# Optimization experiments

Measured on AMD Instinct MI355X. Metric: run time of the kernel, lower is better.

Reference implementation:

```python
import jax, jax.numpy as jnp
import numpy as np

N = 131072        # total points
M = 34            # max_num_neighbors (hard-coded in forward)
K = 15            # kernel points (torch-points3d default for 3D KPConv)
C_IN, C_OUT = 32, 64
POINT_INFLUENCE = 0.04        # prev_grid_size * sigma
KERNEL_RADIUS = 1.5 * POINT_INFLUENCE  # _INFLUENCE_TO_RADIUS * point_influence
BN_EPS = 1e-5
NEG_SLOPE = 0.2


def setup_inputs() -> dict:
    key = jax.random.key(0)
    ks = jax.random.split(key, 6)
    # points in a [0, 0.1]^3 box so random neighbors can fall inside the influence radius
    xyz = jax.random.uniform(ks[0], (N, 3), jnp.float32) * 0.1
    feats = jax.random.normal(ks[1], (N, C_IN), jnp.float32)
    neighbor_idx = jax.random.randint(ks[2], (N, M), 0, N, dtype=jnp.int32)
    # fixed kernel-point disposition: points inside a sphere of radius KERNEL_RADIUS
    kp_dir = jax.random.normal(ks[3], (K, 3), jnp.float32)
    kp_dir = kp_dir / jnp.linalg.norm(kp_dir, axis=1, keepdims=True)
    kp_rad = jax.random.uniform(ks[4], (K, 1), jnp.float32) ** (1.0 / 3.0)
    k_points = kp_dir * kp_rad * KERNEL_RADIUS
    weight = jax.random.normal(ks[5], (K, C_IN, C_OUT), jnp.float32) / np.sqrt(K * C_IN)
    gamma = jnp.ones((C_OUT,), jnp.float32)
    beta = jnp.zeros((C_OUT,), jnp.float32)
    return {"xyz": xyz, "feats": feats, "neighbor_idx": neighbor_idx,
            "weight": weight, "k_points": k_points, "gamma": gamma, "beta": beta}


def _kpconv(xyz, feats, neighbor_idx, weight, k_points):
    # shadow point / shadow feature row for out-of-range neighbor index == N
    sup = jnp.concatenate([xyz, jnp.full((1, 3), 1e6, xyz.dtype)], axis=0)
    f = jnp.concatenate([feats, jnp.zeros((1, feats.shape[1]), feats.dtype)], axis=0)
    # [N, M, 3] neighbor offsets relative to each query point
    nb = sup[neighbor_idx] - xyz[:, None, :]
    # [N, M, K] distance from each neighbor to each kernel point
    diff = nb[:, :, None, :] - k_points[None, None, :, :]
    dist = jnp.sqrt(jnp.sum(diff * diff, axis=-1))
    # linear kernel influence, 'sum' aggregation
    w = jnp.maximum(0.0, 1.0 - dist / POINT_INFLUENCE)          # [N, M, K]
    nb_f = f[neighbor_idx]                                       # [N, M, C_IN]
    wf = jnp.einsum('nmk,nmc->nkc', w, nb_f)                     # [N, K, C_IN]
    return jnp.einsum('nkc,kcd->nd', wf, weight)                 # [N, C_OUT]


def reference(xyz, feats, neighbor_idx, weight, k_points, gamma, beta):
    out = _kpconv(xyz, feats, neighbor_idx, weight, k_points)
    # FastBatchNorm1d (training-mode batch statistics) + LeakyReLU(0.2)
    mean = jnp.mean(out, axis=0)
    var = jnp.mean((out - mean) ** 2, axis=0)
    out = (out - mean) * jax.lax.rsqrt(var + BN_EPS) * gamma + beta
    return jnp.where(out >= 0, out, NEG_SLOPE * out)
```

## Files before the change

### kernel.cpp

```cpp
#include <hip/hip_runtime.h>

#define NPTS 131072
#define MNBR 34
#define KP 15
#define CIN 32
#define COUT 64
#define INV_INFL 25.0f
#define BN_EPS 1e-5f
#define NEG_SLOPE 0.2f
#define PPB 16
#define NBLK (NPTS / PPB)
#define NBIN 512
#define SKIP_D2 0.01f

typedef unsigned short u16;
typedef unsigned int u32;
typedef short short8 __attribute__((ext_vector_type(8)));
typedef float f32x4 __attribute__((ext_vector_type(4)));

static __device__ __forceinline__ u16 f2bf(float f) {
    u32 x = __float_as_uint(f);
    x += 0x7fffu + ((x >> 16) & 1u);
    return (u16)(x >> 16);
}
static __device__ __forceinline__ u32 pk2bf(float lo, float hi) {
    u32 a = __float_as_uint(lo) + 0x8000u;
    u32 b = __float_as_uint(hi) + 0x8000u;
    return (a >> 16) | (b & 0xffff0000u);
}
static __device__ __forceinline__ float rdlanef(float v, int l) {
    return __uint_as_float(__builtin_amdgcn_readlane(__float_as_uint(v), l));
}

#define WS_WT   0u
#define WS_SCSH 65536u
#define WS_SP   131072u
#define WS_QP   262144u
#define WS_XY   393216u
#define WS_FB   2490624u

__global__ __launch_bounds__(256) void prep(const float* __restrict__ Wg,
                                            const float* __restrict__ feats,
                                            const float* __restrict__ xyz,
                                            u16* __restrict__ WT, float4* __restrict__ XY,
                                            u32* __restrict__ FBu, float* __restrict__ SpQp) {
    int b = blockIdx.x;
    if (b < 120) {
        int i2 = b * 256 + threadIdx.x;
        WT[(i2 & 63) * 480 + (i2 >> 6)] = f2bf(Wg[i2]);
    } else if (b < 633) {
        int r = (b - 120) * 256 + threadIdx.x;
        if (r <= NPTS) {
            float4 v;
            if (r < NPTS) v = make_float4(xyz[3 * r], xyz[3 * r + 1], xyz[3 * r + 2], 0.f);
            else          v = make_float4(1e6f, 1e6f, 1e6f, 0.f);
            XY[r] = v;
        }
    } else if (b < 8826) {
        int g = (b - 633) * 256 + threadIdx.x;
        if (g < ((NPTS + 1) * CIN) / 2) {
            int e = g * 2;
            u32 v = 0;
            if (e < NPTS * CIN)
                v = (u32)f2bf(feats[e]) | ((u32)f2bf(feats[e + 1]) << 16);
            FBu[g] = v;
        }
    } else {
        SpQp[(b - 8826) * 256 + threadIdx.x] = 0.f;
    }
}

__global__ __launch_bounds__(128, 3) void kpconv_conv(
    const float* __restrict__ xyz, const int* __restrict__ nbr,
    const float4* __restrict__ XY, const u32* __restrict__ FBu,
    const u16* __restrict__ WT, const float* __restrict__ kpts,
    float* __restrict__ out, float* __restrict__ Sp, float* __restrict__ Qp)
{
    __shared__ u32 wf[PPB * 256];
    __shared__ float4 offs4[2][2][64];

    const int tid = threadIdx.x, lane = tid & 63, wave = tid >> 6;
    const int q = lane >> 4, t = lane & 15;
    const int pbase = blockIdx.x * PPB + wave * 8;

    float axt = 0.f, ayt = 0.f, azt = 0.f, ckt = 1e30f;
    if (t < KP) {
        float kx = kpts[3 * t], ky = kpts[3 * t + 1], kz = kpts[3 * t + 2];
        axt = -2.f * kx; ayt = -2.f * ky; azt = -2.f * kz;
        ckt = fmaf(kx, kx, fmaf(ky, ky, kz * kz));
    }
    const int wslot = (lane & ~7) | ((lane ^ (lane >> 3)) & 7);
    const int sl = q * 8;

    auto ldnbr = [&](int pp) {
        int v = NPTS;
        if (lane < MNBR) v = nbr[(size_t)(pbase + pp) * MNBR + lane];
        if ((u32)v > (u32)NPTS) v = NPTS;
        return v;
    };

    float qxv[8], qyv[8], qzv[8];
    #pragma unroll
    for (int p = 0; p < 8; ++p) {
        const int n1 = pbase + p;
        qxv[p] = xyz[3 * n1]; qyv[p] = xyz[3 * n1 + 1]; qzv[p] = xyz[3 * n1 + 2];
    }

    u32 fbA[8] = {0,0,0,0,0,0,0,0};
    u32 fbB[8] = {0,0,0,0,0,0,0,0};
    u32 fbC[8] = {0,0,0,0,0,0,0,0};
    u32 d32A = 0, d33A = 0, d32B = 0, d33B = 0, d32N = 0, d33N = 0;

    int ix0 = ldnbr(0);
    int ix1 = ldnbr(1);
    int ixF = ldnbr(2);
    int ix3 = ldnbr(3);
    float4 pn0 = XY[ix0];
    float4 pn1 = XY[ix1];
    float4 pnF = XY[ixF];

    {
        float ox = pn0.x - qxv[0], oy = pn0.y - qyv[0], oz = pn0.z - qzv[0];
        float ow = fmaf(ox, ox, fmaf(oy, oy, oz * oz));
        offs4[wave][0][wslot] = make_float4(ox, oy, oz, ow);
        #pragma unroll
        for (int j = 0; j < 8; ++j) {
            float dj = __shfl(ow, sl + j, 64);
            u32 r0 = (u32)__shfl(ix0, sl + j, 64);
            if (dj < SKIP_D2) fbA[j] = FBu[(size_t)r0 * 16 + t];
        }
        float w32 = rdlanef(ow, 32), w33 = rdlanef(ow, 33);
        int r32 = __builtin_amdgcn_readlane(ix0, 32);
        int r33 = __builtin_amdgcn_readlane(ix0, 33);
        if (w32 < SKIP_D2) d32A = FBu[(size_t)r32 * 16 + t];
        if (w33 < SKIP_D2) d33A = FBu[(size_t)r33 * 16 + t];
    }
    float o1x, o1y, o1z, o1w;
    {
        o1x = pn1.x - qxv[1]; o1y = pn1.y - qyv[1]; o1z = pn1.z - qzv[1];
        o1w = fmaf(o1x, o1x, fmaf(o1y, o1y, o1z * o1z));
        #pragma unroll
        for (int j = 0; j < 8; ++j) {
            float dj = __shfl(o1w, sl + j, 64);
            u32 r1 = (u32)__shfl(ix1, sl + j, 64);
            if (dj < SKIP_D2) fbB[j] = FBu[(size_t)r1 * 16 + t];
        }
        float w32 = rdlanef(o1w, 32), w33 = rdlanef(o1w, 33);
        int r32 = __builtin_amdgcn_readlane(ix1, 32);
        int r33 = __builtin_amdgcn_readlane(ix1, 33);
        if (w32 < SKIP_D2) d32B = FBu[(size_t)r32 * 16 + t];
        if (w33 < SKIP_D2) d33B = FBu[(size_t)r33 * 16 + t];
    }

    #pragma unroll
    for (int p = 0; p < 8; ++p) {
        int ixN = NPTS;
        if (p < 4) ixN = ldnbr(p + 4);
        float4 pnN = make_float4(1e6f, 1e6f, 1e6f, 0.f);
        if (p < 5) pnN = XY[ix3];
        float o2x = 0.f, o2y = 0.f, o2z = 0.f, o2w = 1e30f;
        if (p < 6) {
            o2x = pnF.x - qxv[p + 2]; o2y = pnF.y - qyv[p + 2]; o2z = pnF.z - qzv[p + 2];
            o2w = fmaf(o2x, o2x, fmaf(o2y, o2y, o2z * o2z));
            #pragma unroll
            for (int j = 0; j < 8; ++j) {
                float dj = __shfl(o2w, sl + j, 64);
                u32 r2 = (u32)__shfl(ixF, sl + j, 64);
                if (dj < SKIP_D2) fbC[j] = FBu[(size_t)r2 * 16 + t];
            }
            float w32 = rdlanef(o2w, 32), w33 = rdlanef(o2w, 33);
            int r32 = __builtin_amdgcn_readlane(ixF, 32);
            int r33 = __builtin_amdgcn_readlane(ixF, 33);
            if (w32 < SKIP_D2) d32N = FBu[(size_t)r32 * 16 + t];
            if (w33 < SKIP_D2) d33N = FBu[(size_t)r33 * 16 + t];
        }
        if (p < 7) {
            offs4[wave][(p + 1) & 1][wslot] = make_float4(o1x, o1y, o1z, o1w);
        }

        const float4* ob = &offs4[wave][p & 1][0];
        float wj[8];
        #pragma unroll
        for (int j = 0; j < 8; ++j) {
            float4 o = ob[q * 8 + (j ^ q)];
            float d2 = fmaf(o.x, axt, fmaf(o.y, ayt, fmaf(o.z, azt, ckt))) + o.w;
            float dd = __builtin_amdgcn_sqrtf(d2);
            wj[j] = fmaxf(0.f, fmaf(dd, -INV_INFL, 1.f));
        }
        union { short8 v; u32 d[4]; } a1, a2, e1, o1, e2, o2;
        #pragma unroll
        for (int i = 0; i < 4; ++i) a1.d[i] = pk2bf(wj[2 * i], wj[2 * i + 1]);
        {
            float4 oA = ob[36], oB = ob[37];
            float dA = __builtin_amdgcn_sqrtf(fmaf(oA.x, axt, fmaf(oA.y, ayt, fmaf(oA.z, azt, ckt))) + oA.w);
            float dB = __builtin_amdgcn_sqrtf(fmaf(oB.x, axt, fmaf(oB.y, ayt, fmaf(oB.z, azt, ckt))) + oB.w);
            float wA = fmaxf(0.f, fmaf(dA, -INV_INFL, 1.f));
            float wB = fmaxf(0.f, fmaf(dB, -INV_INFL, 1.f));
            a2.d[0] = (q == 0) ? pk2bf(wA, wB) : 0u;
            a2.d[1] = 0; a2.d[2] = 0; a2.d[3] = 0;
        }
        #pragma unroll
        for (int i = 0; i < 4; ++i) {
            u32 aa = fbA[2 * i], bb2 = fbA[2 * i + 1];
            e1.d[i] = (aa & 0xffffu) | (bb2 << 16);
            o1.d[i] = (aa >> 16) | (bb2 & 0xffff0000u);
        }
        {
            u32 lo = (d32A & 0xffffu) | (d33A << 16);
            u32 hi = (d32A >> 16) | (d33A & 0xffff0000u);
            e2.d[0] = (q == 0) ? lo : 0u;  e2.d[1] = 0; e2.d[2] = 0; e2.d[3] = 0;
            o2.d[0] = (q == 0) ? hi : 0u;  o2.d[1] = 0; o2.d[2] = 0; o2.d[3] = 0;
        }
        f32x4 c0 = {0.f, 0.f, 0.f, 0.f}, c1 = {0.f, 0.f, 0.f, 0.f};
        c0 = __builtin_amdgcn_mfma_f32_16x16x32_bf16(a1.v, e1.v, c0, 0, 0, 0);
        c0 = __builtin_amdgcn_mfma_f32_16x16x32_bf16(a2.v, e2.v, c0, 0, 0, 0);
        c1 = __builtin_amdgcn_mfma_f32_16x16x32_bf16(a1.v, o1.v, c1, 0, 0, 0);
        c1 = __builtin_amdgcn_mfma_f32_16x16x32_bf16(a2.v, o2.v, c1, 0, 0, 0);

        const int row = wave * 8 + p;
        #pragma unroll
        for (int r = 0; r < 4; ++r) {
            int ko = q * 4 + r;
            u32 pk = pk2bf(c0[r], c1[r]);
            int unit = ko * 4 + (t >> 2);
            wf[row * 256 + ((unit ^ (row & 7)) << 2) + (t & 3)] = pk;
        }

        #pragma unroll
        for (int j = 0; j < 8; ++j) { fbA[j] = fbB[j]; fbB[j] = fbC[j]; }
        d32A = d32B; d33A = d33B; d32B = d32N; d33B = d33N;
        pnF = pnN; o1x = o2x; o1y = o2y; o1z = o2z; o1w = o2w;
        ixF = ix3; ix3 = ixN;
    }
    __syncthreads();

    const int wcol0 = (wave * 2 + 0) * 16 + t;
    const int wcol1 = (wave * 2 + 1) * 16 + t;
    f32x4 A0 = {0.f, 0.f, 0.f, 0.f}, A1 = {0.f, 0.f, 0.f, 0.f};
    const u16* wt0 = WT + wcol0 * 480 + q * 8;
    const u16* wt1 = WT + wcol1 * 480 + q * 8;
    #pragma unroll
    for (int ks = 0; ks < KP; ++ks) {
        const int u = ks * 4 + q;
        short8 a   = *(const short8*)&wf[t * 256 + ((u ^ (t & 7)) << 2)];
        short8 bb0 = *(const short8*)(wt0 + ks * 32);
        short8 bb1 = *(const short8*)(wt1 + ks * 32);
        A0 = __builtin_amdgcn_mfma_f32_16x16x32_bf16(a, bb0, A0, 0, 0, 0);
        A1 = __builtin_amdgcn_mfma_f32_16x16x32_bf16(a, bb1, A1, 0, 0, 0);
    }
    const int base = blockIdx.x * PPB;
    float s0 = 0.f, q0 = 0.f, s1 = 0.f, q1 = 0.f;
    #pragma unroll
    for (int r = 0; r < 4; ++r) {
        float v0 = A0[r], v1 = A1[r];
        out[(base + q * 4 + r) * COUT + wcol0] = v0;
        out[(base + q * 4 + r) * COUT + wcol1] = v1;
        s0 += v0; q0 = fmaf(v0, v0, q0);
        s1 += v1; q1 = fmaf(v1, v1, q1);
    }
    s0 += __shfl_xor(s0, 16, 64); s0 += __shfl_xor(s0, 32, 64);
    q0 += __shfl_xor(q0, 16, 64); q0 += __shfl_xor(q0, 32, 64);
    s1 += __shfl_xor(s1, 16, 64); s1 += __shfl_xor(s1, 32, 64);
    q1 += __shfl_xor(q1, 16, 64); q1 += __shfl_xor(q1, 32, 64);
    if (q == 0) {
        const int bin = blockIdx.x >> 4;
        atomicAdd(&Sp[wcol0 * NBIN + bin], s0);
        atomicAdd(&Qp[wcol0 * NBIN + bin], q0);
        atomicAdd(&Sp[wcol1 * NBIN + bin], s1);
        atomicAdd(&Qp[wcol1 * NBIN + bin], q1);
    }
}

__global__ __launch_bounds__(256) void bn_reduce(
    const float* __restrict__ Sp, const float* __restrict__ Qp,
    const float* __restrict__ gamma, const float* __restrict__ beta,
    float* __restrict__ scsh)
{
    const int ch = blockIdx.x;
    const int tid = threadIdx.x;
    float s = 0.f, qq = 0.f;
    if (tid < NBIN / 4) {
        float4 a = ((const float4*)(Sp + ch * NBIN))[tid]; s  = a.x + a.y + a.z + a.w;
        float4 b = ((const float4*)(Qp + ch * NBIN))[tid]; qq = b.x + b.y + b.z + b.w;
    }
    #pragma unroll
    for (int off = 1; off < 64; off <<= 1) {
        s += __shfl_xor(s, off, 64); qq += __shfl_xor(qq, off, 64);
    }
    __shared__ float red[8];
    const int w = tid >> 6;
    if ((tid & 63) == 0) { red[w * 2] = s; red[w * 2 + 1] = qq; }
    __syncthreads();
    if (tid == 0) {
        s  = red[0] + red[2] + red[4] + red[6];
        qq = red[1] + red[3] + red[5] + red[7];
        float mean = s * (1.0f / NPTS);
        float var  = qq * (1.0f / NPTS) - mean * mean;
        float sc = gamma[ch] * rsqrtf(var + BN_EPS);
        scsh[ch] = sc;
        scsh[64 + ch] = beta[ch] - mean * sc;
    }
}

__global__ __launch_bounds__(256) void bn_apply(
    float* __restrict__ out, const float* __restrict__ scsh)
{
    __shared__ float sc[64], sh[64];
    const int tid = threadIdx.x;
    if (tid < 64) { sc[tid] = scsh[tid]; sh[tid] = scsh[64 + tid]; }
    __syncthreads();
    const int gid = blockIdx.x * 256 + tid;
    float4 v = ((const float4*)out)[gid];
    const int c0 = (gid * 4) & 63;
    float y0 = fmaf(v.x, sc[c0 + 0], sh[c0 + 0]);
    float y1 = fmaf(v.y, sc[c0 + 1], sh[c0 + 1]);
    float y2 = fmaf(v.z, sc[c0 + 2], sh[c0 + 2]);
    float y3 = fmaf(v.w, sc[c0 + 3], sh[c0 + 3]);
    float4 w;
    w.x = fmaxf(y0, NEG_SLOPE * y0);
    w.y = fmaxf(y1, NEG_SLOPE * y1);
    w.z = fmaxf(y2, NEG_SLOPE * y2);
    w.w = fmaxf(y3, NEG_SLOPE * y3);
    ((float4*)out)[gid] = w;
}

extern "C" void kernel_launch(void* const* d_in, const int* in_sizes, int n_in,
                              void* d_out, int out_size, void* d_ws, size_t ws_size,
                              hipStream_t stream) {
    (void)in_sizes; (void)n_in; (void)out_size; (void)ws_size;
    const float* xyz   = (const float*)d_in[0];
    const float* feats = (const float*)d_in[1];
    const int*   nbr   = (const int*)d_in[2];
    const float* Wg    = (const float*)d_in[3];
    const float* kpts  = (const float*)d_in[4];
    const float* gamma = (const float*)d_in[5];
    const float* beta  = (const float*)d_in[6];
    float* out = (float*)d_out;
    char* ws = (char*)d_ws;
    u16*    WT   = (u16*)(ws + WS_WT);
    float*  scsh = (float*)(ws + WS_SCSH);
    float*  Sp   = (float*)(ws + WS_SP);
    float*  Qp   = (float*)(ws + WS_QP);
    float4* XY   = (float4*)(ws + WS_XY);
    u32*    FBu  = (u32*)(ws + WS_FB);

    prep<<<dim3(9082), dim3(256), 0, stream>>>(Wg, feats, xyz, WT, XY, FBu, Sp);
    kpconv_conv<<<dim3(NBLK), dim3(128), 0, stream>>>(xyz, nbr, XY, FBu, WT, kpts, out, Sp, Qp);
    bn_reduce<<<dim3(64), dim3(256), 0, stream>>>(Sp, Qp, gamma, beta, scsh);
    bn_apply<<<dim3((NPTS * COUT) / (256 * 4)), dim3(256), 0, stream>>>(out, scsh);
}
```

Baseline: 226.1 us.

## Replace per-block stat atomics with separate partial-sum kernel and vectorize feature conversion

Removes the per-block atomicAdd of batch-norm sums and sums of squares from the conv kernel. A new stat_partial kernel re-reads the conv output and writes deterministic per-block partials, which bn_reduce then sums. The prep kernel now converts features to bf16 with float4 loads and uint2 stores, and it no longer has to zero the atomic bins. The cost is one extra kernel launch and a second full pass over the 32 MB output in exchange for removing atomic contention from the conv epilogue.

```diff
diff --git a/kernel.cpp b/kernel.cpp
--- a/kernel.cpp
+++ b/kernel.cpp
@@ -10,7 +10,7 @@
 #define NEG_SLOPE 0.2f
 #define PPB 16
 #define NBLK (NPTS / PPB)
-#define NBIN 512
+#define NSB 512
 #define SKIP_D2 0.01f
 
 typedef unsigned short u16;
@@ -34,8 +34,7 @@
 
 #define WS_WT   0u
 #define WS_SCSH 65536u
-#define WS_SP   131072u
-#define WS_QP   262144u
+#define WS_PART 131072u
 #define WS_XY   393216u
 #define WS_FB   2490624u
 
@@ -43,7 +42,7 @@
                                             const float* __restrict__ feats,
                                             const float* __restrict__ xyz,
                                             u16* __restrict__ WT, float4* __restrict__ XY,
-                                            u32* __restrict__ FBu, float* __restrict__ SpQp) {
+                                            uint2* __restrict__ FB2) {
     int b = blockIdx.x;
     if (b < 120) {
         int i2 = b * 256 + threadIdx.x;
@@ -56,17 +55,17 @@
             else          v = make_float4(1e6f, 1e6f, 1e6f, 0.f);
             XY[r] = v;
         }
-    } else if (b < 8826) {
-        int g = (b - 633) * 256 + threadIdx.x;
-        if (g < ((NPTS + 1) * CIN) / 2) {
-            int e = g * 2;
-            u32 v = 0;
-            if (e < NPTS * CIN)
-                v = (u32)f2bf(feats[e]) | ((u32)f2bf(feats[e + 1]) << 16);
-            FBu[g] = v;
-        }
     } else {
-        SpQp[(b - 8826) * 256 + threadIdx.x] = 0.f;
+        int g2 = (b - 633) * 256 + threadIdx.x;
+        if (g2 < 1048584) {
+            uint2 v = make_uint2(0u, 0u);
+            if (g2 < 1048576) {
+                float4 f = ((const float4*)feats)[g2];
+                v.x = (u32)f2bf(f.x) | ((u32)f2bf(f.y) << 16);
+                v.y = (u32)f2bf(f.z) | ((u32)f2bf(f.w) << 16);
+            }
+            FB2[g2] = v;
+        }
     }
 }
 
@@ -74,7 +73,7 @@
     const float* __restrict__ xyz, const int* __restrict__ nbr,
     const float4* __restrict__ XY, const u32* __restrict__ FBu,
     const u16* __restrict__ WT, const float* __restrict__ kpts,
-    float* __restrict__ out, float* __restrict__ Sp, float* __restrict__ Qp)
+    float* __restrict__ out)
 {
     __shared__ u32 wf[PPB * 256];
     __shared__ float4 offs4[2][2][64];
@@ -187,7 +186,7 @@
             float dd = __builtin_amdgcn_sqrtf(d2);
             wj[j] = fmaxf(0.f, fmaf(dd, -INV_INFL, 1.f));
         }
-        union { short8 v; u32 d[4]; } a1, a2, e1, o1, e2, o2;
+        union { short8 v; u32 d[4]; } a1, a2, e1, o1u, e2, o2u;
         #pragma unroll
         for (int i = 0; i < 4; ++i) a1.d[i] = pk2bf(wj[2 * i], wj[2 * i + 1]);
         {
@@ -203,19 +202,19 @@
         for (int i = 0; i < 4; ++i) {
             u32 aa = fbA[2 * i], bb2 = fbA[2 * i + 1];
             e1.d[i] = (aa & 0xffffu) | (bb2 << 16);
-            o1.d[i] = (aa >> 16) | (bb2 & 0xffff0000u);
+            o1u.d[i] = (aa >> 16) | (bb2 & 0xffff0000u);
         }
         {
             u32 lo = (d32A & 0xffffu) | (d33A << 16);
             u32 hi = (d32A >> 16) | (d33A & 0xffff0000u);
             e2.d[0] = (q == 0) ? lo : 0u;  e2.d[1] = 0; e2.d[2] = 0; e2.d[3] = 0;
-            o2.d[0] = (q == 0) ? hi : 0u;  o2.d[1] = 0; o2.d[2] = 0; o2.d[3] = 0;
+            o2u.d[0] = (q == 0) ? hi : 0u; o2u.d[1] = 0; o2u.d[2] = 0; o2u.d[3] = 0;
         }
         f32x4 c0 = {0.f, 0.f, 0.f, 0.f}, c1 = {0.f, 0.f, 0.f, 0.f};
         c0 = __builtin_amdgcn_mfma_f32_16x16x32_bf16(a1.v, e1.v, c0, 0, 0, 0);
         c0 = __builtin_amdgcn_mfma_f32_16x16x32_bf16(a2.v, e2.v, c0, 0, 0, 0);
-        c1 = __builtin_amdgcn_mfma_f32_16x16x32_bf16(a1.v, o1.v, c1, 0, 0, 0);
-        c1 = __builtin_amdgcn_mfma_f32_16x16x32_bf16(a2.v, o2.v, c1, 0, 0, 0);
+        c1 = __builtin_amdgcn_mfma_f32_16x16x32_bf16(a1.v, o1u.v, c1, 0, 0, 0);
+        c1 = __builtin_amdgcn_mfma_f32_16x16x32_bf16(a2.v, o2u.v, c1, 0, 0, 0);
 
         const int row = wave * 8 + p;
         #pragma unroll
@@ -249,39 +248,65 @@
         A1 = __builtin_amdgcn_mfma_f32_16x16x32_bf16(a, bb1, A1, 0, 0, 0);
     }
     const int base = blockIdx.x * PPB;
-    float s0 = 0.f, q0 = 0.f, s1 = 0.f, q1 = 0.f;
     #pragma unroll
     for (int r = 0; r < 4; ++r) {
-        float v0 = A0[r], v1 = A1[r];
-        out[(base + q * 4 + r) * COUT + wcol0] = v0;
-        out[(base + q * 4 + r) * COUT + wcol1] = v1;
-        s0 += v0; q0 = fmaf(v0, v0, q0);
-        s1 += v1; q1 = fmaf(v1, v1, q1);
+        out[(base + q * 4 + r) * COUT + wcol0] = A0[r];
+        out[(base + q * 4 + r) * COUT + wcol1] = A1[r];
+    }
+}
+
+__global__ __launch_bounds__(256) void stat_partial(const float* __restrict__ out,
+                                                    float* __restrict__ Part)
+{
+    const int tid = threadIdx.x, lane = tid & 63, wave = tid >> 6;
+    const int u = tid & 15;
+    const int pr = tid >> 4;
+    const float4* O = (const float4*)out + (size_t)blockIdx.x * 4096;
+    float s0 = 0.f, s1 = 0.f, s2 = 0.f, s3 = 0.f;
+    float q0 = 0.f, q1 = 0.f, q2 = 0.f, q3 = 0.f;
+    #pragma unroll
+    for (int it = 0; it < 16; ++it) {
+        float4 v = O[(it * 16 + pr) * 16 + u];
+        s0 += v.x; q0 = fmaf(v.x, v.x, q0);
+        s1 += v.y; q1 = fmaf(v.y, v.y, q1);
+        s2 += v.z; q2 = fmaf(v.z, v.z, q2);
+        s3 += v.w; q3 = fmaf(v.w, v.w, q3);
     }
     s0 += __shfl_xor(s0, 16, 64); s0 += __shfl_xor(s0, 32, 64);
+    s1 += __shfl_xor(s1, 16, 64); s1 += __shfl_xor(s1, 32, 64);
+    s2 += __shfl_xor(s2, 16, 64); s2 += __shfl_xor(s2, 32, 64);
+    s3 += __shfl_xor(s3, 16, 64); s3 += __shfl_xor(s3, 32, 64);
     q0 += __shfl_xor(q0, 16, 64); q0 += __shfl_xor(q0, 32, 64);
-    s1 += __shfl_xor(s1, 16, 64); s1 += __shfl_xor(s1, 32, 64);
     q1 += __shfl_xor(q1, 16, 64); q1 += __shfl_xor(q1, 32, 64);
-    if (q == 0) {
-        const int bin = blockIdx.x >> 4;
-        atomicAdd(&Sp[wcol0 * NBIN + bin], s0);
-        atomicAdd(&Qp[wcol0 * NBIN + bin], q0);
-        atomicAdd(&Sp[wcol1 * NBIN + bin], s1);
-        atomicAdd(&Qp[wcol1 * NBIN + bin], q1);
+    q2 += __shfl_xor(q2, 16, 64); q2 += __shfl_xor(q2, 32, 64);
+    q3 += __shfl_xor(q3, 16, 64); q3 += __shfl_xor(q3, 32, 64);
+    __shared__ float red[4][16][8];
+    if (lane < 16) {
+        float* r = red[wave][lane];
+        r[0] = s0; r[1] = s1; r[2] = s2; r[3] = s3;
+        r[4] = q0; r[5] = q1; r[6] = q2; r[7] = q3;
+    }
+    __syncthreads();
+    if (tid < 128) {
+        int ch = tid >> 1, su = tid & 1;
+        int uu = ch >> 2, c = ch & 3;
+        float v = red[0][uu][su * 4 + c] + red[1][uu][su * 4 + c]
+                + red[2][uu][su * 4 + c] + red[3][uu][su * 4 + c];
+        Part[blockIdx.x * 128 + tid] = v;
     }
 }
 
 __global__ __launch_bounds__(256) void bn_reduce(
-    const float* __restrict__ Sp, const float* __restrict__ Qp,
+    const float* __restrict__ Part,
     const float* __restrict__ gamma, const float* __restrict__ beta,
     float* __restrict__ scsh)
 {
     const int ch = blockIdx.x;
     const int tid = threadIdx.x;
     float s = 0.f, qq = 0.f;
-    if (tid < NBIN / 4) {
-        float4 a = ((const float4*)(Sp + ch * NBIN))[tid]; s  = a.x + a.y + a.z + a.w;
-        float4 b = ((const float4*)(Qp + ch * NBIN))[tid]; qq = b.x + b.y + b.z + b.w;
+    for (int b = tid; b < NSB; b += 256) {
+        s  += Part[b * 128 + ch * 2];
+        qq += Part[b * 128 + ch * 2 + 1];
     }
     #pragma unroll
     for (int off = 1; off < 64; off <<= 1) {
@@ -339,13 +364,13 @@
     char* ws = (char*)d_ws;
     u16*    WT   = (u16*)(ws + WS_WT);
     float*  scsh = (float*)(ws + WS_SCSH);
-    float*  Sp   = (float*)(ws + WS_SP);
-    float*  Qp   = (float*)(ws + WS_QP);
+    float*  Part = (float*)(ws + WS_PART);
     float4* XY   = (float4*)(ws + WS_XY);
     u32*    FBu  = (u32*)(ws + WS_FB);
 
-    prep<<<dim3(9082), dim3(256), 0, stream>>>(Wg, feats, xyz, WT, XY, FBu, Sp);
-    kpconv_conv<<<dim3(NBLK), dim3(128), 0, stream>>>(xyz, nbr, XY, FBu, WT, kpts, out, Sp, Qp);
-    bn_reduce<<<dim3(64), dim3(256), 0, stream>>>(Sp, Qp, gamma, beta, scsh);
+    prep<<<dim3(4730), dim3(256), 0, stream>>>(Wg, feats, xyz, WT, XY, (uint2*)FBu);
+    kpconv_conv<<<dim3(NBLK), dim3(128), 0, stream>>>(xyz, nbr, XY, FBu, WT, kpts, out);
+    stat_partial<<<dim3(NSB), dim3(256), 0, stream>>>(out, Part);
+    bn_reduce<<<dim3(64), dim3(256), 0, stream>>>(Part, gamma, beta, scsh);
     bn_apply<<<dim3((NPTS * COUT) / (256 * 4)), dim3(256), 0, stream>>>(out, scsh);
 }
```

Measured after the change: 220.8 us. 2.3% less time.
